# Kernel tuning notes

Hardware: AMD Instinct MI355X
Metric: run time of the kernel (lower is better)

The kernel has to match this reference:

```python
import jax, jax.numpy as jnp
import numpy as np

N_NODES = 50000
N_EDGES = 800000
F_IN = 128
HIDDEN = 256
N_GRAPHS = 128


def setup_inputs() -> dict:
    key = jax.random.key(0)
    ks = jax.random.split(key, 13)
    x = jax.random.normal(ks[0], (N_NODES, F_IN), dtype=jnp.float32)
    edge_src = jax.random.randint(ks[1], (N_EDGES,), 0, N_NODES, dtype=jnp.int32)
    edge_dst = jax.random.randint(ks[2], (N_EDGES,), 0, N_NODES, dtype=jnp.int32)
    edge_w = jax.random.uniform(ks[3], (N_EDGES,), dtype=jnp.float32)
    seg_ids = jnp.sort(jax.random.randint(ks[4], (N_NODES,), 0, N_GRAPHS, dtype=jnp.int32))
    def lin(k, fan_in, fan_out):
        s = 1.0 / np.sqrt(fan_in)
        return jax.random.uniform(k, (fan_in, fan_out), dtype=jnp.float32, minval=-s, maxval=s)
    W1 = lin(ks[5], F_IN, HIDDEN);  b1 = jnp.zeros((HIDDEN,), jnp.float32)
    W2 = lin(ks[6], HIDDEN, HIDDEN); b2 = jnp.zeros((HIDDEN,), jnp.float32)
    Wd = lin(ks[7], HIDDEN, HIDDEN); bd = jnp.zeros((HIDDEN,), jnp.float32)
    Wo = lin(ks[8], HIDDEN, 1);      bo = jnp.zeros((1,), jnp.float32)
    return {"x": x, "edge_src": edge_src, "edge_dst": edge_dst, "edge_w": edge_w,
            "seg_ids": seg_ids, "W1": W1, "b1": b1, "W2": W2, "b2": b2,
            "Wd": Wd, "bd": bd, "Wo": Wo, "bo": bo}


def reference(x, edge_src, edge_dst, edge_w, seg_ids, W1, b1, W2, b2, Wd, bd, Wo, bo):
    n_nodes = x.shape[0]

    def spmm(h):
        # sparse A_norm @ h via gather-scale-scatter over the edge list
        msg = h[edge_src] * edge_w[:, None]            # [E, H]
        return jax.ops.segment_sum(msg, edge_dst, num_segments=n_nodes)

    # GCNConv 1: relu(A @ X @ W1 + b1); dropout p=0 is identity
    h = jax.nn.relu(spmm(x @ W1) + b1)                 # [N, H]
    # GCNConv 2
    h = jax.nn.relu(spmm(h @ W2) + b2)                 # [N, H]
    # GlobalSumPool keyed by graph index
    g = jax.ops.segment_sum(h, seg_ids, num_segments=N_GRAPHS)  # [G, H]
    # dense head
    g = jax.nn.relu(g @ Wd + bd)
    return g @ Wo + bo                                 # [G, 1]
```

## Files before the change

### kernel.cpp

```cpp
#include <hip/hip_runtime.h>
#include <hip/hip_bf16.h>


typedef short v8s __attribute__((ext_vector_type(8)));
typedef float v4f __attribute__((ext_vector_type(4)));
typedef float v2f __attribute__((ext_vector_type(2)));

#define BKT_CAP 6144

__device__ inline unsigned bf16u(float f) {
    unsigned u = __builtin_bit_cast(unsigned, f);
    return (u + 0x7fffu + ((u >> 16) & 1u)) >> 16;
}
__device__ inline float bflo(unsigned v) { return __builtin_bit_cast(float, v << 16); }
__device__ inline float bfhi(unsigned v) { return __builtin_bit_cast(float, v & 0xffff0000u); }

__global__ __launch_bounds__(256) void prep(
    const float* __restrict__ x, unsigned char* __restrict__ x8,
    const float* __restrict__ W1, ushort* __restrict__ Wt1,
    const float* __restrict__ W2, ushort* __restrict__ Wt2)
{
    int b = blockIdx.x;
    int t = threadIdx.x;
    if (b < 6250) {
        int i = b * 256 + t;
        if (i < 1600000) {
            float4 v = ((const float4*)x)[i];
            int pk = __builtin_amdgcn_cvt_pk_fp8_f32(v.x, v.y, 0, false);
            pk = __builtin_amdgcn_cvt_pk_fp8_f32(v.z, v.w, pk, true);
            ((unsigned*)x8)[i] = (unsigned)pk;
        }
    } else if (b < 6506) {
        int n = b - 6250;
        if (t < 128) Wt1[n * 128 + t] = (ushort)bf16u(W1[t * 256 + n]);
    } else {
        int n = b - 6506;
        Wt2[n * 256 + t] = (ushort)bf16u(W2[t * 256 + n]);
    }
}

__global__ __launch_bounds__(256) void bin_pass(
    const int* __restrict__ src, const int* __restrict__ dst,
    const float* __restrict__ w, int* __restrict__ bcnt,
    uint2* __restrict__ stage, float* __restrict__ g, int E)
{
    __shared__ int hist[256];
    __shared__ int excl[256];
    __shared__ int gbase[256];
    __shared__ uint2 stg[2048];

    int t = threadIdx.x, b = blockIdx.x;
    if (b < 128) g[b * 256 + t] = 0.f;

    int e0 = b * 2048;
    hist[t] = 0;
    __syncthreads();

    int d_[8]; unsigned pk_[8]; int rk_[8]; int bk_[8];
    #pragma unroll
    for (int j = 0; j < 8; j++) {
        int e = e0 + t + j * 256;
        if (e < E) {
            int d = dst[e];
            d_[j] = d;
            bk_[j] = d >> 8;
            pk_[j] = (unsigned)src[e] | (bf16u(w[e]) << 16);
            rk_[j] = atomicAdd(&hist[bk_[j]], 1);
        } else d_[j] = -1;
    }
    __syncthreads();

    int cnt = hist[t];
    excl[t] = cnt;
    __syncthreads();
    for (int o = 1; o < 256; o <<= 1) {
        int v = (t >= o) ? excl[t - o] : 0;
        __syncthreads();
        excl[t] += v;
        __syncthreads();
    }
    int ex = excl[t] - cnt;
    if (cnt > 0) gbase[t] = atomicAdd(&bcnt[t], cnt);
    __syncthreads();
    excl[t] = ex;
    __syncthreads();

    #pragma unroll
    for (int j = 0; j < 8; j++)
        if (d_[j] >= 0)
            stg[excl[bk_[j]] + rk_[j]] = make_uint2(pk_[j], (unsigned)d_[j]);
    __syncthreads();

    int nval = min(2048, E - e0);
    #pragma unroll
    for (int j = 0; j < 8; j++) {
        int sidx = t + j * 256;
        if (sidx < nval) {
            uint2 ent = stg[sidx];
            int bk = (int)(ent.y >> 8);
            stage[(size_t)bk * BKT_CAP + gbase[bk] + sidx - excl[bk]] = ent;
        }
    }
}

__global__ __launch_bounds__(256) void sort_build(
    const uint2* __restrict__ stage, const int* __restrict__ bcnt,
    unsigned* __restrict__ edges, int* __restrict__ off, int N, int E)
{
    __shared__ unsigned sorted[BKT_CAP];
    __shared__ int hist[256];
    __shared__ int s[256];
    __shared__ int cur[256];
    __shared__ int psum[4];
    __shared__ int sbase;

    int t = threadIdx.x, b = blockIdx.x;
    const uint2* reg = stage + (size_t)b * BKT_CAP;
    int cnt = bcnt[b];

    int pred = (t < b) ? bcnt[t] : 0;
    #pragma unroll
    for (int o = 32; o > 0; o >>= 1) pred += __shfl_down(pred, o, 64);
    if ((t & 63) == 0) psum[t >> 6] = pred;
    hist[t] = 0;
    __syncthreads();
    if (t == 0) sbase = psum[0] + psum[1] + psum[2] + psum[3];

    for (int i = t; i < cnt; i += 256)
        atomicAdd(&hist[reg[i].y & 255u], 1);
    __syncthreads();

    int h = hist[t];
    s[t] = h;
    __syncthreads();
    for (int o = 1; o < 256; o <<= 1) {
        int v = (t >= o) ? s[t - o] : 0;
        __syncthreads();
        s[t] += v;
        __syncthreads();
    }
    int ex = s[t] - h;
    cur[t] = ex;
    __syncthreads();

    int nn = b * 256 + t;
    if (nn <= N) off[nn] = sbase + ex;

    for (int i = t; i < cnt; i += 256) {
        uint2 ent = reg[i];
        int r = atomicAdd(&cur[ent.y & 255u], 1);
        sorted[r] = ent.x;
    }
    __syncthreads();
    for (int i = t; i < cnt; i += 256)
        edges[sbase + i] = sorted[i];
}

__global__ __launch_bounds__(256) void spmm128(
    const unsigned char* __restrict__ x8, const int* __restrict__ off,
    const unsigned* __restrict__ edges, ushort* __restrict__ S, int n)
{
    int node = blockIdx.x * 4 + (threadIdx.x >> 6);
    if (node >= n) return;
    int lane = threadIdx.x & 63;
    const ushort* base = (const ushort*)x8;
    int e0 = off[node], e1 = off[node + 1];
    float a0 = 0.f, a1 = 0.f;
    int e = e0;
    for (; e + 4 <= e1; e += 4) {
        unsigned ed0 = edges[e],     ed1 = edges[e + 1];
        unsigned ed2 = edges[e + 2], ed3 = edges[e + 3];
        float w0 = bfhi(ed0), w1 = bfhi(ed1);
        float w2 = bfhi(ed2), w3 = bfhi(ed3);
        ushort v0 = base[(size_t)(ed0 & 0xffffu) * 64 + lane];
        ushort v1 = base[(size_t)(ed1 & 0xffffu) * 64 + lane];
        ushort v2 = base[(size_t)(ed2 & 0xffffu) * 64 + lane];
        ushort v3 = base[(size_t)(ed3 & 0xffffu) * 64 + lane];
        v2f f0 = __builtin_amdgcn_cvt_pk_f32_fp8((int)v0, false);
        v2f f1 = __builtin_amdgcn_cvt_pk_f32_fp8((int)v1, false);
        v2f f2 = __builtin_amdgcn_cvt_pk_f32_fp8((int)v2, false);
        v2f f3 = __builtin_amdgcn_cvt_pk_f32_fp8((int)v3, false);
        a0 += f0.x * w0 + f1.x * w1 + f2.x * w2 + f3.x * w3;
        a1 += f0.y * w0 + f1.y * w1 + f2.y * w2 + f3.y * w3;
    }
    for (; e < e1; e++) {
        unsigned ed = edges[e];
        float w0 = bfhi(ed);
        ushort v0 = base[(size_t)(ed & 0xffffu) * 64 + lane];
        v2f f0 = __builtin_amdgcn_cvt_pk_f32_fp8((int)v0, false);
        a0 += f0.x * w0;
        a1 += f0.y * w0;
    }
    ((unsigned*)S)[(size_t)node * 64 + lane] = (bf16u(a1) << 16) | bf16u(a0);
}

__global__ __launch_bounds__(256) void spmm256(
    const unsigned char* __restrict__ h8, const int* __restrict__ off,
    const unsigned* __restrict__ edges, ushort* __restrict__ S, int n)
{
    int node = blockIdx.x * 4 + (threadIdx.x >> 6);
    if (node >= n) return;
    int lane = threadIdx.x & 63;
    const unsigned* base = (const unsigned*)h8;
    int e0 = off[node], e1 = off[node + 1];
    float a0 = 0.f, a1 = 0.f, a2 = 0.f, a3 = 0.f;
    int e = e0;
    for (; e + 4 <= e1; e += 4) {
        unsigned ed0 = edges[e],     ed1 = edges[e + 1];
        unsigned ed2 = edges[e + 2], ed3 = edges[e + 3];
        float w0 = bfhi(ed0), w1 = bfhi(ed1);
        float w2 = bfhi(ed2), w3 = bfhi(ed3);
        unsigned v0 = base[(size_t)(ed0 & 0xffffu) * 64 + lane];
        unsigned v1 = base[(size_t)(ed1 & 0xffffu) * 64 + lane];
        unsigned v2 = base[(size_t)(ed2 & 0xffffu) * 64 + lane];
        unsigned v3 = base[(size_t)(ed3 & 0xffffu) * 64 + lane];
        v2f l0 = __builtin_amdgcn_cvt_pk_f32_fp8((int)v0, false);
        v2f h0 = __builtin_amdgcn_cvt_pk_f32_fp8((int)v0, true);
        v2f l1 = __builtin_amdgcn_cvt_pk_f32_fp8((int)v1, false);
        v2f h1v = __builtin_amdgcn_cvt_pk_f32_fp8((int)v1, true);
        v2f l2 = __builtin_amdgcn_cvt_pk_f32_fp8((int)v2, false);
        v2f h2 = __builtin_amdgcn_cvt_pk_f32_fp8((int)v2, true);
        v2f l3 = __builtin_amdgcn_cvt_pk_f32_fp8((int)v3, false);
        v2f h3 = __builtin_amdgcn_cvt_pk_f32_fp8((int)v3, true);
        a0 += l0.x * w0 + l1.x * w1 + l2.x * w2 + l3.x * w3;
        a1 += l0.y * w0 + l1.y * w1 + l2.y * w2 + l3.y * w3;
        a2 += h0.x * w0 + h1v.x * w1 + h2.x * w2 + h3.x * w3;
        a3 += h0.y * w0 + h1v.y * w1 + h2.y * w2 + h3.y * w3;
    }
    for (; e < e1; e++) {
        unsigned ed = edges[e];
        float w0 = bfhi(ed);
        unsigned v0 = base[(size_t)(ed & 0xffffu) * 64 + lane];
        v2f l0 = __builtin_amdgcn_cvt_pk_f32_fp8((int)v0, false);
        v2f h0 = __builtin_amdgcn_cvt_pk_f32_fp8((int)v0, true);
        a0 += l0.x * w0;
        a1 += l0.y * w0;
        a2 += h0.x * w0;
        a3 += h0.y * w0;
    }
    uint2 o;
    o.x = (bf16u(a1) << 16) | bf16u(a0);
    o.y = (bf16u(a3) << 16) | bf16u(a2);
    ((uint2*)S)[(size_t)node * 64 + lane] = o;
}

template <int K, int OFMT, bool POOL>
__global__ __launch_bounds__(512) void gemm_tile(
    const ushort* __restrict__ A, const ushort* __restrict__ Wt,
    const float* __restrict__ bias, void* __restrict__ out,
    const int* __restrict__ seg, float* __restrict__ g, int M)
{
    __shared__ __align__(16) ushort As[128 * 32];
    __shared__ __align__(16) ushort Bs[256 * 32];
    __shared__ int segsh[128];

    const int tid = threadIdx.x;
    const int bm = blockIdx.x * 128;
    const int wave = tid >> 6, lane = tid & 63;
    const int wm = wave >> 2, wn = wave & 3;
    const int r = lane & 15, q = lane >> 4;

    if (POOL && tid < 128) {
        int gr = bm + tid;
        segsh[tid] = (gr < M) ? seg[gr] : 0x7fffffff;
    }

    const int o0 = tid * 16;
    const int row0 = o0 >> 6;
    const int kb0 = o0 & 63;

    const char* Ab = (const char*)A;
    const char* Bb = (const char*)Wt;

    uint4 ra0, rb0, rb1;
    ra0 = *(const uint4*)(Ab + ((size_t)(bm + row0) * K) * 2 + kb0);
    rb0 = *(const uint4*)(Bb + ((size_t)(row0)       * K) * 2 + kb0);
    rb1 = *(const uint4*)(Bb + ((size_t)(row0 + 128) * K) * 2 + kb0);

    v4f acc[4][4];
    #pragma unroll
    for (int i = 0; i < 4; i++)
        #pragma unroll
        for (int j = 0; j < 4; j++) acc[i][j] = (v4f){0.f, 0.f, 0.f, 0.f};

    const int NK = K / 32;
    for (int ks = 0; ks < NK; ks++) {
        __syncthreads();
        *(uint4*)((char*)As + o0)        = ra0;
        *(uint4*)((char*)Bs + o0)        = rb0;
        *(uint4*)((char*)Bs + o0 + 8192) = rb1;
        if (ks + 1 < NK) {
            const int kof = (ks + 1) * 64;
            ra0 = *(const uint4*)(Ab + ((size_t)(bm + row0) * K) * 2 + kof + kb0);
            rb0 = *(const uint4*)(Bb + ((size_t)(row0)       * K) * 2 + kof + kb0);
            rb1 = *(const uint4*)(Bb + ((size_t)(row0 + 128) * K) * 2 + kof + kb0);
        }
        __syncthreads();

        v8s af[4], bf[4];
        #pragma unroll
        for (int i = 0; i < 4; i++)
            af[i] = *(const v8s*)(As + (wm * 64 + i * 16 + r) * 32 + q * 8);
        #pragma unroll
        for (int j = 0; j < 4; j++)
            bf[j] = *(const v8s*)(Bs + (wn * 64 + j * 16 + r) * 32 + q * 8);
        #pragma unroll
        for (int i = 0; i < 4; i++)
            #pragma unroll
            for (int j = 0; j < 4; j++)
                acc[i][j] = __builtin_amdgcn_mfma_f32_16x16x32_bf16(
                    af[i], bf[j], acc[i][j], 0, 0, 0);
    }

    if constexpr (POOL) {
        #pragma unroll
        for (int j = 0; j < 4; j++) {
            float b = bias[wn * 64 + j * 16 + r];
            #pragma unroll
            for (int i = 0; i < 4; i++)
                #pragma unroll
                for (int ii = 0; ii < 4; ii++)
                    acc[i][j][ii] = fmaxf(acc[i][j][ii] + b, 0.f);
        }
        int myseg[16];
        #pragma unroll
        for (int i = 0; i < 4; i++)
            #pragma unroll
            for (int ii = 0; ii < 4; ii++)
                myseg[i * 4 + ii] = segsh[wm * 64 + i * 16 + q * 4 + ii];
        int s_lo = segsh[0];
        int s_hi = segsh[min(127, M - 1 - bm)];
        for (int s = s_lo; s <= s_hi; s++) {
            #pragma unroll
            for (int j = 0; j < 4; j++) {
                float p = 0.f;
                #pragma unroll
                for (int i = 0; i < 4; i++)
                    #pragma unroll
                    for (int ii = 0; ii < 4; ii++)
                        if (myseg[i * 4 + ii] == s) p += acc[i][j][ii];
                p += __shfl_xor(p, 16, 64);
                p += __shfl_xor(p, 32, 64);
                if (lane < 16)
                    atomicAdd(&g[s * 256 + wn * 64 + j * 16 + r], p);
            }
        }
    } else {
        #pragma unroll
        for (int j = 0; j < 4; j++) {
            int col = wn * 64 + j * 16 + r;
            float b = bias[col];
            #pragma unroll
            for (int i = 0; i < 4; i++) {
                #pragma unroll
                for (int ii = 0; ii < 4; ii++) {
                    int row = bm + wm * 64 + i * 16 + q * 4 + ii;
                    if (row < M) {
                        float v = fmaxf(acc[i][j][ii] + b, 0.f);
                        if constexpr (OFMT == 1) {
                            ((ushort*)out)[(size_t)row * 256 + col] = (ushort)bf16u(v);
                        } else if constexpr (OFMT == 2) {
                            unsigned pk = (unsigned)__builtin_amdgcn_cvt_pk_fp8_f32(
                                v, v, 0, false);
                            ((unsigned char*)out)[(size_t)row * 256 + col] =
                                (unsigned char)(pk & 0xffu);
                        } else {
                            ((float*)out)[(size_t)row * 256 + col] = v;
                        }
                    }
                }
            }
        }
    }
}

__global__ __launch_bounds__(256) void head(
    const float* __restrict__ g, const float* __restrict__ Wd,
    const float* __restrict__ bd, const float* __restrict__ Wo,
    const float* __restrict__ bo, float* __restrict__ out)
{
    __shared__ float gr[256];
    int j = threadIdx.x;
    int gi = blockIdx.x;
    gr[j] = g[(size_t)gi * 256 + j];
    __syncthreads();
    float a2 = bd[j];
    for (int k = 0; k < 256; k++)
        a2 += gr[k] * Wd[(size_t)k * 256 + j];
    a2 = fmaxf(a2, 0.f);

    float v = a2 * Wo[j];
    #pragma unroll
    for (int off = 32; off > 0; off >>= 1)
        v += __shfl_down(v, off, 64);
    __shared__ float partial[4];
    if ((j & 63) == 0) partial[j >> 6] = v;
    __syncthreads();
    if (j == 0)
        out[gi] = partial[0] + partial[1] + partial[2] + partial[3] + bo[0];
}

extern "C" void kernel_launch(void* const* d_in, const int* in_sizes, int n_in,
                              void* d_out, int out_size, void* d_ws, size_t ws_size,
                              hipStream_t stream) {
    const float* x   = (const float*)d_in[0];
    const int*   esrc= (const int*)  d_in[1];
    const int*   edst= (const int*)  d_in[2];
    const float* ew  = (const float*)d_in[3];
    const int*   seg = (const int*)  d_in[4];
    const float* W1  = (const float*)d_in[5];
    const float* b1  = (const float*)d_in[6];
    const float* W2  = (const float*)d_in[7];
    const float* b2  = (const float*)d_in[8];
    const float* Wd  = (const float*)d_in[9];
    const float* bd  = (const float*)d_in[10];
    const float* Wo  = (const float*)d_in[11];
    const float* bo  = (const float*)d_in[12];
    float* out = (float*)d_out;

    const int N = 50000, E = 800000, G = 128, H = 256, F = 128;
    const int NPAD = 50048;
    const int NB = (N + 255) / 256;

    char* p = (char*)d_ws;
    char* region0 = p;                  p += (size_t)N * H * sizeof(float);
    unsigned char* x8 = (unsigned char*)region0;
    ushort* S1 = (ushort*)(region0 + (size_t)N * F);
    uint2* stage = (uint2*)(region0 + (size_t)32 * 1024 * 1024);
    unsigned char* h8 = (unsigned char*)p;
                                        p += (size_t)N * H;
    ushort* S2 = (ushort*)p;            p += (size_t)NPAD * H * sizeof(ushort);
    float* g   = (float*)p;             p += (size_t)G * H * sizeof(float);
    int*   bcnt= (int*)p;               p += 256 * sizeof(int);
    int*   off = (int*)p;               p += (size_t)(N + 1) * sizeof(int) + 12;
    unsigned* edges=(unsigned*)p;       p += (size_t)E * sizeof(unsigned);
    ushort* Wt1= (ushort*)p;            p += (size_t)H * F * sizeof(ushort);
    ushort* Wt2= (ushort*)p;            p += (size_t)H * H * sizeof(ushort);

    hipMemsetAsync(bcnt, 0, 256 * sizeof(int), stream);
    prep<<<6762, 256, 0, stream>>>(x, x8, W1, Wt1, W2, Wt2);
    bin_pass<<<(E + 2047) / 2048, 256, 0, stream>>>(esrc, edst, ew, bcnt, stage, g, E);
    sort_build<<<NB, 256, 0, stream>>>(stage, bcnt, edges, off, N, E);

    spmm128<<<(N + 3) / 4, 256, 0, stream>>>(x8, off, edges, S1, N);
    gemm_tile<128, 2, false><<<NPAD / 128, 512, 0, stream>>>(
        S1, Wt1, b1, h8, nullptr, nullptr, N);

    spmm256<<<(N + 3) / 4, 256, 0, stream>>>(h8, off, edges, S2, N);
    gemm_tile<256, 0, true><<<NPAD / 128, 512, 0, stream>>>(
        S2, Wt2, b2, nullptr, seg, g, N);

    head<<<G, 256, 0, stream>>>(g, Wd, bd, Wo, bo, out);
}
```

Baseline: 240.4 us.

## Slice feature columns across blocks and split edges across lane groups in SpMM

Replaces the two per-node SpMM kernels with one templated kernel. Each block now handles a feature slice of 16 dwords for 16 nodes. Within a wave, four lane groups each take a different edge and combine their partial sums with cross-lane shuffles. The aim is to raise memory-level parallelism per wave and to keep each block's gathered slice small, so that blocks on the same slice share cache reuse through interleaved block ordering. The cost is extra shuffle reductions, predicated tail loads, and a larger grid that re-reads the edge lists once per slice.

```diff
diff --git a/kernel.cpp b/kernel.cpp
--- a/kernel.cpp
+++ b/kernel.cpp
@@ -156,92 +156,62 @@
         edges[sbase + i] = sorted[i];
 }
 
-__global__ __launch_bounds__(256) void spmm128(
-    const unsigned char* __restrict__ x8, const int* __restrict__ off,
-    const unsigned* __restrict__ edges, ushort* __restrict__ S, int n)
-{
-    int node = blockIdx.x * 4 + (threadIdx.x >> 6);
-    if (node >= n) return;
+template <int ROWU, int SLICES>
+__global__ __launch_bounds__(256) void spmm_sliced(
+    const unsigned* __restrict__ base, const int* __restrict__ off,
+    const unsigned* __restrict__ edges, uint2* __restrict__ S, int n)
+{
+    int bid = blockIdx.x;
+    int sl, ng;
+    if (SLICES == 4) { sl = (bid & 7) >> 1; ng = (bid >> 3) * 2 + (bid & 1); }
+    else             { sl = (bid & 7) >> 2; ng = (bid >> 3) * 4 + (bid & 3); }
+    int wid = threadIdx.x >> 6;
     int lane = threadIdx.x & 63;
-    const ushort* base = (const ushort*)x8;
-    int e0 = off[node], e1 = off[node + 1];
-    float a0 = 0.f, a1 = 0.f;
-    int e = e0;
-    for (; e + 4 <= e1; e += 4) {
-        unsigned ed0 = edges[e],     ed1 = edges[e + 1];
-        unsigned ed2 = edges[e + 2], ed3 = edges[e + 3];
-        float w0 = bfhi(ed0), w1 = bfhi(ed1);
-        float w2 = bfhi(ed2), w3 = bfhi(ed3);
-        ushort v0 = base[(size_t)(ed0 & 0xffffu) * 64 + lane];
-        ushort v1 = base[(size_t)(ed1 & 0xffffu) * 64 + lane];
-        ushort v2 = base[(size_t)(ed2 & 0xffffu) * 64 + lane];
-        ushort v3 = base[(size_t)(ed3 & 0xffffu) * 64 + lane];
-        v2f f0 = __builtin_amdgcn_cvt_pk_f32_fp8((int)v0, false);
-        v2f f1 = __builtin_amdgcn_cvt_pk_f32_fp8((int)v1, false);
-        v2f f2 = __builtin_amdgcn_cvt_pk_f32_fp8((int)v2, false);
-        v2f f3 = __builtin_amdgcn_cvt_pk_f32_fp8((int)v3, false);
-        a0 += f0.x * w0 + f1.x * w1 + f2.x * w2 + f3.x * w3;
-        a1 += f0.y * w0 + f1.y * w1 + f2.y * w2 + f3.y * w3;
-    }
-    for (; e < e1; e++) {
-        unsigned ed = edges[e];
-        float w0 = bfhi(ed);
-        ushort v0 = base[(size_t)(ed & 0xffffu) * 64 + lane];
-        v2f f0 = __builtin_amdgcn_cvt_pk_f32_fp8((int)v0, false);
-        a0 += f0.x * w0;
-        a1 += f0.y * w0;
-    }
-    ((unsigned*)S)[(size_t)node * 64 + lane] = (bf16u(a1) << 16) | bf16u(a0);
-}
-
-__global__ __launch_bounds__(256) void spmm256(
-    const unsigned char* __restrict__ h8, const int* __restrict__ off,
-    const unsigned* __restrict__ edges, ushort* __restrict__ S, int n)
-{
-    int node = blockIdx.x * 4 + (threadIdx.x >> 6);
-    if (node >= n) return;
-    int lane = threadIdx.x & 63;
-    const unsigned* base = (const unsigned*)h8;
-    int e0 = off[node], e1 = off[node + 1];
-    float a0 = 0.f, a1 = 0.f, a2 = 0.f, a3 = 0.f;
-    int e = e0;
-    for (; e + 4 <= e1; e += 4) {
-        unsigned ed0 = edges[e],     ed1 = edges[e + 1];
-        unsigned ed2 = edges[e + 2], ed3 = edges[e + 3];
-        float w0 = bfhi(ed0), w1 = bfhi(ed1);
-        float w2 = bfhi(ed2), w3 = bfhi(ed3);
-        unsigned v0 = base[(size_t)(ed0 & 0xffffu) * 64 + lane];
-        unsigned v1 = base[(size_t)(ed1 & 0xffffu) * 64 + lane];
-        unsigned v2 = base[(size_t)(ed2 & 0xffffu) * 64 + lane];
-        unsigned v3 = base[(size_t)(ed3 & 0xffffu) * 64 + lane];
-        v2f l0 = __builtin_amdgcn_cvt_pk_f32_fp8((int)v0, false);
-        v2f h0 = __builtin_amdgcn_cvt_pk_f32_fp8((int)v0, true);
-        v2f l1 = __builtin_amdgcn_cvt_pk_f32_fp8((int)v1, false);
-        v2f h1v = __builtin_amdgcn_cvt_pk_f32_fp8((int)v1, true);
-        v2f l2 = __builtin_amdgcn_cvt_pk_f32_fp8((int)v2, false);
-        v2f h2 = __builtin_amdgcn_cvt_pk_f32_fp8((int)v2, true);
-        v2f l3 = __builtin_amdgcn_cvt_pk_f32_fp8((int)v3, false);
-        v2f h3 = __builtin_amdgcn_cvt_pk_f32_fp8((int)v3, true);
-        a0 += l0.x * w0 + l1.x * w1 + l2.x * w2 + l3.x * w3;
-        a1 += l0.y * w0 + l1.y * w1 + l2.y * w2 + l3.y * w3;
-        a2 += h0.x * w0 + h1v.x * w1 + h2.x * w2 + h3.x * w3;
-        a3 += h0.y * w0 + h1v.y * w1 + h2.y * w2 + h3.y * w3;
-    }
-    for (; e < e1; e++) {
-        unsigned ed = edges[e];
-        float w0 = bfhi(ed);
-        unsigned v0 = base[(size_t)(ed & 0xffffu) * 64 + lane];
-        v2f l0 = __builtin_amdgcn_cvt_pk_f32_fp8((int)v0, false);
-        v2f h0 = __builtin_amdgcn_cvt_pk_f32_fp8((int)v0, true);
-        a0 += l0.x * w0;
-        a1 += l0.y * w0;
-        a2 += h0.x * w0;
-        a3 += h0.y * w0;
-    }
-    uint2 o;
-    o.x = (bf16u(a1) << 16) | bf16u(a0);
-    o.y = (bf16u(a3) << 16) | bf16u(a2);
-    ((uint2*)S)[(size_t)node * 64 + lane] = o;
+    int ej = lane >> 4, fi = lane & 15;
+    int slo = sl * 16 + fi;
+
+    #pragma unroll
+    for (int i = 0; i < 4; i++) {
+        int node = ng * 16 + wid * 4 + i;
+        if (node >= n) continue;
+        int e0 = off[node], e1 = off[node + 1];
+        float a0 = 0.f, a1 = 0.f, a2 = 0.f, a3 = 0.f;
+        for (int e = e0; e < e1; e += 16) {
+            unsigned ed[4]; float w[4]; unsigned v[4];
+            #pragma unroll
+            for (int g = 0; g < 4; g++) {
+                int eg = e + g * 4 + ej;
+                ed[g] = (eg < e1) ? edges[eg] : 0u;
+            }
+            #pragma unroll
+            for (int g = 0; g < 4; g++) {
+                int eg = e + g * 4 + ej;
+                w[g] = (eg < e1) ? bfhi(ed[g]) : 0.f;
+            }
+            #pragma unroll
+            for (int g = 0; g < 4; g++)
+                v[g] = base[(size_t)(ed[g] & 0xffffu) * ROWU + slo];
+            #pragma unroll
+            for (int g = 0; g < 4; g++) {
+                v2f l = __builtin_amdgcn_cvt_pk_f32_fp8((int)v[g], false);
+                v2f h = __builtin_amdgcn_cvt_pk_f32_fp8((int)v[g], true);
+                a0 += l.x * w[g];
+                a1 += l.y * w[g];
+                a2 += h.x * w[g];
+                a3 += h.y * w[g];
+            }
+        }
+        a0 += __shfl_xor(a0, 16, 64); a0 += __shfl_xor(a0, 32, 64);
+        a1 += __shfl_xor(a1, 16, 64); a1 += __shfl_xor(a1, 32, 64);
+        a2 += __shfl_xor(a2, 16, 64); a2 += __shfl_xor(a2, 32, 64);
+        a3 += __shfl_xor(a3, 16, 64); a3 += __shfl_xor(a3, 32, 64);
+        if (ej == 0) {
+            uint2 o;
+            o.x = (bf16u(a1) << 16) | bf16u(a0);
+            o.y = (bf16u(a3) << 16) | bf16u(a2);
+            S[(size_t)node * ROWU + slo] = o;
+        }
+    }
 }
 
 template <int K, int OFMT, bool POOL>
@@ -442,11 +412,13 @@
     bin_pass<<<(E + 2047) / 2048, 256, 0, stream>>>(esrc, edst, ew, bcnt, stage, g, E);
     sort_build<<<NB, 256, 0, stream>>>(stage, bcnt, edges, off, N, E);
 
-    spmm128<<<(N + 3) / 4, 256, 0, stream>>>(x8, off, edges, S1, N);
+    spmm_sliced<32, 2><<<6256, 256, 0, stream>>>(
+        (const unsigned*)x8, off, edges, (uint2*)S1, N);
     gemm_tile<128, 2, false><<<NPAD / 128, 512, 0, stream>>>(
         S1, Wt1, b1, h8, nullptr, nullptr, N);
 
-    spmm256<<<(N + 3) / 4, 256, 0, stream>>>(h8, off, edges, S2, N);
+    spmm_sliced<64, 4><<<12504, 256, 0, stream>>>(
+        (const unsigned*)h8, off, edges, (uint2*)S2, N);
     gemm_tile<256, 0, true><<<NPAD / 128, 512, 0, stream>>>(
         S2, Wt2, b2, nullptr, seg, g, N);
 
```

New measurement: 254.4 us. 5.8% more time.
